# Kernel optimization log

Measured on AMD Instinct MI355X. Metric: run time of the kernel, lower is better.

## Reference

```python
import jax, jax.numpy as jnp
import numpy as np

B, N, D = 256, 128, 512
NUM_TYPES, NUM_STATS = 6, 8
W_TYPE, W_STATS, W_CORR = 1.0, 1.0, 0.5
LN_EPS = 1e-5


def setup_inputs() -> dict:
    key = jax.random.key(0)
    ks = jax.random.split(key, 20)
    s = 1.0 / np.sqrt(D)
    inp = {
        "column_embeddings": jax.random.normal(ks[0], (B, N, D), jnp.float32),
        "masked_columns": jax.random.bernoulli(ks[1], 0.15, (B, N)),
        "type_targets": jax.random.randint(ks[2], (N,), 0, NUM_TYPES),
        "column_statistics": jax.random.normal(ks[3], (B, N, NUM_STATS), jnp.float32),
        "column_correlations": jnp.tanh(jax.random.normal(ks[4], (B, N, N), jnp.float32)),
        # type head: Linear(D,D) -> GELU -> LayerNorm -> Linear(D,NUM_TYPES)
        "t_W1": jax.random.normal(ks[5], (D, D), jnp.float32) * s,
        "t_b1": jnp.zeros((D,), jnp.float32),
        "t_g": jnp.ones((D,), jnp.float32),
        "t_beta": jnp.zeros((D,), jnp.float32),
        "t_W2": jax.random.normal(ks[6], (D, NUM_TYPES), jnp.float32) * s,
        "t_b2": jnp.zeros((NUM_TYPES,), jnp.float32),
        # stats head
        "s_W1": jax.random.normal(ks[7], (D, D), jnp.float32) * s,
        "s_b1": jnp.zeros((D,), jnp.float32),
        "s_g": jnp.ones((D,), jnp.float32),
        "s_beta": jnp.zeros((D,), jnp.float32),
        "s_W2": jax.random.normal(ks[8], (D, NUM_STATS), jnp.float32) * s,
        "s_b2": jnp.zeros((NUM_STATS,), jnp.float32),
        # bilinear correlation: x_i^T W x_j + b
        "c_W": jax.random.normal(ks[9], (D, D), jnp.float32) * s,
        "c_b": jnp.zeros((), jnp.float32),
    }
    return inp


def _mlp_head(x, W1, b1, g, beta, W2, b2):
    h = jax.nn.gelu(x @ W1 + b1, approximate=False)
    mu = h.mean(-1, keepdims=True)
    var = ((h - mu) ** 2).mean(-1, keepdims=True)
    h = (h - mu) * jax.lax.rsqrt(var + LN_EPS) * g + beta
    return h @ W2 + b2


def _forward(column_embeddings, masked_columns, type_targets,
             column_statistics, column_correlations,
             t_W1, t_b1, t_g, t_beta, t_W2, t_b2,
             s_W1, s_b1, s_g, s_beta, s_W2, s_b2,
             c_W, c_b):
    e = column_embeddings  # [B,N,D]
    type_logits = _mlp_head(e, t_W1, t_b1, t_g, t_beta, t_W2, t_b2)   # [B,N,T]
    stats_preds = _mlp_head(e, s_W1, s_b1, s_g, s_beta, s_W2, s_b2)   # [B,N,S]

    # batched bilinear correlation: tanh(e_i W e_j + b), diag forced to 1
    u = jnp.einsum('bnd,de->bne', e, c_W)            # [B,N,D]
    corr = jnp.tanh(jnp.einsum('bne,bme->bnm', u, e) + c_b)  # [B,N,N]
    eye = jnp.eye(e.shape[1], dtype=corr.dtype)
    corr = corr * (1.0 - eye) + eye

    m = masked_columns.astype(jnp.float32)           # [B,N]
    n_masked = jnp.maximum(m.sum(), 1.0)

    # type loss: masked-mean cross entropy; targets broadcast over batch
    logp = jax.nn.log_softmax(type_logits, axis=-1)
    tgt = jnp.broadcast_to(type_targets[None, :], m.shape)
    ce = -jnp.take_along_axis(logp, tgt[..., None], axis=-1)[..., 0]  # [B,N]
    type_loss = (ce * m).sum() / n_masked

    # stats loss: masked-mean MSE over [B,N,S]
    se = (stats_preds - column_statistics) ** 2
    stats_loss = (se * m[..., None]).sum() / (n_masked * se.shape[-1])

    # correlation loss: mask_expanded = m_i | m_j
    me = jnp.maximum(m[:, :, None], m[:, None, :])   # [B,N,N]
    n_me = jnp.maximum(me.sum(), 1.0)
    ce2 = (corr - column_correlations) ** 2
    correlation_loss = (ce2 * me).sum() / n_me

    total = W_TYPE * type_loss + W_STATS * stats_loss + W_CORR * correlation_loss
    return total


def reference(column_embeddings, masked_columns, type_targets,
              column_statistics, column_correlations,
              t_W1, t_b1, t_g, t_beta, t_W2, t_b2,
              s_W1, s_b1, s_g, s_beta, s_W2, s_b2,
              c_W, c_b):
    return _forward(column_embeddings, masked_columns, type_targets,
                    column_statistics, column_correlations,
                    t_W1, t_b1, t_g, t_beta, t_W2, t_b2,
                    s_W1, s_b1, s_g, s_beta, s_W2, s_b2,
                    c_W, c_b)
```

## Files before the change

kernel.cpp:

```cpp
#include <hip/hip_runtime.h>
#include <math.h>

#define Bx 256
#define Nx 128
#define Dx 512
#define NTYPES 6
#define NSTATS 8
#define LN_EPS 1e-5f
#define CAP 8192

typedef __attribute__((ext_vector_type(8))) short frag8;
typedef __attribute__((ext_vector_type(4))) float f32x4;

__device__ __forceinline__ unsigned short f2bf(float f) {
    unsigned u = __float_as_uint(f);
    u += 0x7fff + ((u >> 16) & 1);
    return (unsigned short)(u >> 16);
}
__device__ __forceinline__ float bf2f(unsigned short s) {
    return __uint_as_float((unsigned)s << 16);
}

#define ASYNC16(g, l) __builtin_amdgcn_global_load_lds(                      \
    (const __attribute__((address_space(1))) void*)(g),                      \
    (__attribute__((address_space(3))) void*)(l), 16, 0, 0)

#define VWAIT(NIMM)                                                          \
    asm volatile("s_waitcnt vmcnt(" #NIMM ")" ::: "memory");                 \
    __builtin_amdgcn_sched_barrier(0);
#define BARX __builtin_amdgcn_s_barrier();

#define EB_OFF    0ULL
#define HC_OFF    33554432ULL
#define WT_OFF    67108864ULL
#define WTC_OFF   68157440ULL
#define WC_OFF    68681728ULL
#define LIST_OFF  69206016ULL
#define CNTS_OFF  69238784ULL
#define BASES_OFF 69239808ULL
#define CNTP_OFF  69240832ULL
#define ACC_OFF   69240848ULL
#define DONE_OFF  69240864ULL

__global__ __launch_bounds__(256) void k_prep(
    const float* __restrict__ e, const float* __restrict__ W0,
    const float* __restrict__ W1, const float* __restrict__ W2,
    unsigned short* __restrict__ Eb, unsigned short* __restrict__ Tcmb,
    unsigned short* __restrict__ Tc, unsigned short* __restrict__ Wc,
    const int* __restrict__ m, int* __restrict__ list,
    int* __restrict__ cnts, int* __restrict__ bases, int* cntp) {
    const int bid = blockIdx.x;
    const int t = threadIdx.x;
    if (bid < 256) {
        const int b = bid;
        const int r = b * Nx + t;
        int v = 0;
        if (t < 128) v = (m[r] != 0) ? 1 : 0;
        const unsigned long long bal = __ballot(v);
        const int wid = t >> 6, lane = t & 63;
        __shared__ int wcnt[2];
        __shared__ int base;
        if (lane == 0 && wid < 2) wcnt[wid] = __popcll(bal);
        __syncthreads();
        const int cnt = wcnt[0] + wcnt[1];
        if (t == 0) {
            base = atomicAdd(cntp, cnt);
            cnts[b] = cnt;
            bases[b] = base;
        }
        __syncthreads();
        if (t < 128 && v) {
            const int rank = __popcll(bal & ((1ULL << lane) - 1)) +
                             (wid ? wcnt[0] : 0);
            const int p = base + rank;
            if (p < CAP) list[p] = r;
        }
        return;
    }
    if (bid < 448) {
        const int lin = bid - 256;
        const int mid = lin >> 6;
        const int tl  = lin & 63;
        const int ti = tl >> 3, tj = tl & 7;
        const float* W = (mid == 0) ? W0 : (mid == 1) ? W1 : W2;
        unsigned short* T = (mid == 2) ? Tc : (Tcmb + mid * 262144);
        __shared__ float sh[64][65];
        const int c = t & 63;
        const int r4 = t >> 6;
#pragma unroll
        for (int rr = 0; rr < 16; ++rr) {
            const int row = rr * 4 + r4;
            sh[row][c] = W[(size_t)(ti * 64 + row) * Dx + tj * 64 + c];
        }
        __syncthreads();
#pragma unroll
        for (int rr = 0; rr < 16; ++rr) {
            const int col2 = rr * 4 + r4;
            T[(size_t)(tj * 64 + col2) * Dx + ti * 64 + c] = f2bf(sh[c][col2]);
        }
        return;
    }
    if (bid < 512) {
        const int base = (bid - 448) * 4096 + t * 16;
        const float4* src = (const float4*)(W2 + base);
        unsigned short o[16];
#pragma unroll
        for (int q = 0; q < 4; ++q) {
            const float4 v = src[q];
            o[q * 4 + 0] = f2bf(v.x); o[q * 4 + 1] = f2bf(v.y);
            o[q * 4 + 2] = f2bf(v.z); o[q * 4 + 3] = f2bf(v.w);
        }
        *(uint4*)(Wc + base) = *(const uint4*)(o);
        *(uint4*)(Wc + base + 8) = *(const uint4*)(o + 8);
        return;
    }
    const int r = (bid - 512) * 4 + (t >> 6);
    const int lane = t & 63;
    const float4* src = (const float4*)(e + (size_t)r * Dx);
    const float4 a = src[lane * 2];
    const float4 b = src[lane * 2 + 1];
    unsigned short u[8] = {f2bf(a.x), f2bf(a.y), f2bf(a.z), f2bf(a.w),
                           f2bf(b.x), f2bf(b.y), f2bf(b.z), f2bf(b.w)};
    ((uint4*)(Eb + (size_t)r * Dx))[lane] = *(const uint4*)u;
}

__global__ __launch_bounds__(512) void k_gemms(
    const unsigned short* __restrict__ Eb,
    const unsigned short* __restrict__ Wtcmb,
    const unsigned short* __restrict__ Wtc,
    const unsigned short* __restrict__ Wc,
    const float* __restrict__ bias0, const float* __restrict__ bias1,
    unsigned short* __restrict__ Hc,
    const int* __restrict__ list, const int* __restrict__ cntp) {
    __shared__ unsigned short As[2 * 4096];
    __shared__ unsigned short Bs[2 * 8192];
    const int bid = blockIdx.x;
    const int t = threadIdx.x;
    const int cnt = min(*cntp, CAP);
    const int rt = ((bid >> 6) << 3) | (bid & 7);
    const int row0 = rt << 7;
    if (row0 >= cnt) return;
    const int ct = (bid >> 3) & 7;
    const int col0 = ct << 8;
    const unsigned short* Bbase =
        (ct < 4) ? (Wtcmb + (size_t)ct * 256 * Dx)
      : (ct < 6) ? (Wtc + (size_t)(ct - 4) * 256 * Dx)
                 : (Wc + (size_t)(ct - 6) * 256 * Dx);
    const int kq = (t & 3) ^ ((t >> 3) & 3);
    const int ra = list[min(row0 + (t >> 2), cnt - 1)];
    const unsigned short* pA = Eb + (size_t)ra * Dx + kq * 8;
    const unsigned short* pB0 = Bbase + (size_t)(t >> 2) * Dx + kq * 8;
    const unsigned short* pB1 = pB0 + (size_t)128 * Dx;
    const int w = t >> 6, l = t & 63;
    const int wr = (w >> 2) * 64, wcol = (w & 3) * 64;
    const int quad = l >> 4, mr = l & 15;
    const int co = (quad ^ ((mr >> 1) & 3)) * 8;

#define MSTAGE(bf, k0)                                                       \
  { ASYNC16(pA + (k0), As + (bf) * 4096 + t * 8);                            \
    ASYNC16(pB0 + (k0), Bs + (bf) * 8192 + t * 8);                           \
    ASYNC16(pB1 + (k0), Bs + (bf) * 8192 + 4096 + t * 8); }

    f32x4 acc[4][4] = {};
    MSTAGE(0, 0);
    int buf = 0;
    for (int k = 0; k < 16; ++k) {
        if (k < 15) { MSTAGE(buf ^ 1, (k + 1) * 32); VWAIT(3); }
        else        { VWAIT(0); }
        BARX;
        frag8 af[4], bfv[4];
#pragma unroll
        for (int i = 0; i < 4; ++i)
            af[i] = *(const frag8*)&As[buf * 4096 + (wr + i * 16 + mr) * 32 + co];
#pragma unroll
        for (int j = 0; j < 4; ++j)
            bfv[j] = *(const frag8*)&Bs[buf * 8192 + (wcol + j * 16 + mr) * 32 + co];
        __builtin_amdgcn_s_setprio(1);
#pragma unroll
        for (int i = 0; i < 4; ++i)
#pragma unroll
            for (int j = 0; j < 4; ++j)
                acc[i][j] = __builtin_amdgcn_mfma_f32_16x16x32_bf16(
                    af[i], bfv[j], acc[i][j], 0, 0, 0);
        __builtin_amdgcn_s_setprio(0);
        if (k < 15) BARX;
        buf ^= 1;
    }
#pragma unroll
    for (int i = 0; i < 4; ++i)
#pragma unroll
        for (int j = 0; j < 4; ++j)
#pragma unroll
            for (int r = 0; r < 4; ++r) {
                const int row = row0 + wr + i * 16 + quad * 4 + r;
                const int col = col0 + wcol + j * 16 + mr;
                float v = acc[i][j][r];
                if (col < 1024) {
                    v += (col < 512) ? bias0[col] : bias1[col - 512];
                    v = 0.5f * v * (1.0f + erff(v * 0.70710678118654752f));
                }
                Hc[(size_t)row * 2048 + col] = f2bf(v);
            }
#undef MSTAGE
}

__global__ __launch_bounds__(256) void k_tail(
    const unsigned short* __restrict__ Eb,
    const float* __restrict__ Ct, const int* __restrict__ m,
    const float* __restrict__ cbp,
    const unsigned short* __restrict__ Hc,
    const float* __restrict__ tg, const float* __restrict__ tbeta,
    const float* __restrict__ tW2, const float* __restrict__ tb2,
    const float* __restrict__ sg, const float* __restrict__ sbeta,
    const float* __restrict__ sW2, const float* __restrict__ sb2,
    const int* __restrict__ list, const int* __restrict__ cnts,
    const int* __restrict__ bases, const int* __restrict__ cntp,
    const int* __restrict__ tgt, const float* __restrict__ stats,
    float* __restrict__ accs, int* __restrict__ done,
    float* __restrict__ out) {
    __shared__ unsigned short Elds[2 * 4096];
    __shared__ unsigned short Ulds[2 * 4096];
    __shared__ unsigned short Vlds[2 * 4096];
    __shared__ float mloc[128];
    __shared__ int lrow[128];
    __shared__ float redf[4][2];
    const int t = threadIdx.x;
    const int w = t >> 6, l = t & 63;
    const int quad = l >> 4, mr = l & 15;

    if (blockIdx.x < 256) {
        const int b = blockIdx.x;
        const int cnt = cnts[b];
        const int cbase = bases[b];
        const int nt = (cnt + 15) >> 4;
        if (t < 128) {
            mloc[t] = (m[b * Nx + t] != 0) ? 1.0f : 0.0f;
            lrow[t] = (t < cnt) ? (list[cbase + t] & (Nx - 1)) : 0;
        }
        __syncthreads();
        float T1 = 0.0f, T2 = 0.0f, Tov = 0.0f;
        if (cnt > 0) {
            const int kq = (t & 3) ^ ((t >> 3) & 3);
            const size_t rb = (size_t)b * Nx;
            const unsigned short* pE0 = Eb + (rb + (t >> 2)) * Dx + kq * 8;
            const unsigned short* pE1 = Eb + (rb + 64 + (t >> 2)) * Dx + kq * 8;
            const int ur0 = min((t >> 2), cnt - 1);
            const int ur1 = min(64 + (t >> 2), cnt - 1);
            const unsigned short* pU0 = Hc + (size_t)(cbase + ur0) * 2048 + 1024 + kq * 8;
            const unsigned short* pU1 = Hc + (size_t)(cbase + ur1) * 2048 + 1024 + kq * 8;
            const unsigned short* pV0 = Hc + (size_t)(cbase + ur0) * 2048 + 1536 + kq * 8;
            const unsigned short* pV1 = Hc + (size_t)(cbase + ur1) * 2048 + 1536 + kq * 8;
            const int co = (quad ^ ((mr >> 1) & 3)) * 8;

#define CSTAGE(bf, k0)                                                       \
  { ASYNC16(pE0 + (k0), Elds + (bf) * 4096 + t * 8);                         \
    ASYNC16(pE1 + (k0), Elds + (bf) * 4096 + 2048 + t * 8);                  \
    ASYNC16(pU0 + (k0), Ulds + (bf) * 4096 + t * 8);                         \
    ASYNC16(pU1 + (k0), Ulds + (bf) * 4096 + 2048 + t * 8);                  \
    ASYNC16(pV0 + (k0), Vlds + (bf) * 4096 + t * 8);                         \
    ASYNC16(pV1 + (k0), Vlds + (bf) * 4096 + 2048 + t * 8); }

            f32x4 ar[8][2] = {};
            f32x4 ac[2][8] = {};
            CSTAGE(0, 0);
            int buf = 0;
            for (int k = 0; k < 16; ++k) {
                if (k < 15) { CSTAGE(buf ^ 1, (k + 1) * 32); VWAIT(6); }
                else        { VWAIT(0); }
                BARX;
                frag8 ef[2];
#pragma unroll
                for (int eidx = 0; eidx < 2; ++eidx)
                    ef[eidx] = *(const frag8*)&Elds[buf * 4096 +
                        (w * 32 + eidx * 16 + mr) * 32 + co];
                __builtin_amdgcn_s_setprio(1);
#pragma unroll
                for (int it = 0; it < 8; ++it)
                    if (it < nt) {
                        const frag8 uf = *(const frag8*)&Ulds[buf * 4096 +
                            (it * 16 + mr) * 32 + co];
                        ar[it][0] = __builtin_amdgcn_mfma_f32_16x16x32_bf16(
                            uf, ef[0], ar[it][0], 0, 0, 0);
                        ar[it][1] = __builtin_amdgcn_mfma_f32_16x16x32_bf16(
                            uf, ef[1], ar[it][1], 0, 0, 0);
                    }
#pragma unroll
                for (int jt = 0; jt < 8; ++jt)
                    if (jt < nt) {
                        const frag8 vf = *(const frag8*)&Vlds[buf * 4096 +
                            (jt * 16 + mr) * 32 + co];
                        ac[0][jt] = __builtin_amdgcn_mfma_f32_16x16x32_bf16(
                            ef[0], vf, ac[0][jt], 0, 0, 0);
                        ac[1][jt] = __builtin_amdgcn_mfma_f32_16x16x32_bf16(
                            ef[1], vf, ac[1][jt], 0, 0, 0);
                    }
                __builtin_amdgcn_s_setprio(0);
                if (k < 15) BARX;
                buf ^= 1;
            }
            const float cb = cbp[0];
            const float* Ctb = Ct + (size_t)b * Nx * Nx;
#pragma unroll
            for (int it = 0; it < 8; ++it)
                if (it < nt) {
#pragma unroll
                    for (int eidx = 0; eidx < 2; ++eidx) {
                        const int j = w * 32 + eidx * 16 + mr;
#pragma unroll
                        for (int r = 0; r < 4; ++r) {
                            const int pos = it * 16 + quad * 4 + r;
                            if (pos < cnt) {
                                const int i = lrow[pos];
                                const float s = ar[it][eidx][r];
                                const float c = (i == j) ? 1.0f : tanhf(s + cb);
                                const float d = c - Ctb[i * Nx + j];
                                T1 += d * d;
                                Tov += d * d * mloc[j];
                            }
                        }
                    }
                }
#pragma unroll
            for (int jt = 0; jt < 8; ++jt)
                if (jt < nt) {
                    const int pos = jt * 16 + mr;
                    const int valid = (pos < cnt);
                    const int j = lrow[pos];
#pragma unroll
                    for (int eidx = 0; eidx < 2; ++eidx) {
#pragma unroll
                        for (int r = 0; r < 4; ++r) {
                            if (valid) {
                                const int i = w * 32 + eidx * 16 + quad * 4 + r;
                                const float s = ac[eidx][jt][r];
                                const float c = (i == j) ? 1.0f : tanhf(s + cb);
                                const float d = c - Ctb[i * Nx + j];
                                T2 += d * d;
                            }
                        }
                    }
                }
#undef CSTAGE
        }
        float lsum = T1 + T2 - Tov;
#pragma unroll
        for (int off = 32; off > 0; off >>= 1) lsum += __shfl_down(lsum, off);
        if (l == 0) redf[w][0] = lsum;
        __syncthreads();
        if (t == 0) {
            atomicAdd(&accs[2], redf[0][0] + redf[1][0] + redf[2][0] + redf[3][0]);
            const float c = (float)cnt;
            atomicAdd(&accs[3], 256.0f * c - c * c);
        }
    } else {
        const int blk = blockIdx.x - 256;
        const int cnt = min(*cntp, CAP);
        float ce_acc = 0.0f, sse_acc = 0.0f;
        for (int idx = blk * 4 + w; idx < cnt; idx += 256 * 4) {
            const int r = list[idx];
            const uint4 ut = ((const uint4*)(Hc + (size_t)idx * 2048))[l];
            const uint4 us = ((const uint4*)(Hc + (size_t)idx * 2048 + 512))[l];
            float a[8], b8[8];
            {
                const unsigned uu[4] = {ut.x, ut.y, ut.z, ut.w};
                const unsigned vv[4] = {us.x, us.y, us.z, us.w};
#pragma unroll
                for (int j = 0; j < 4; ++j) {
                    a[2 * j]      = bf2f((unsigned short)(uu[j] & 0xffff));
                    a[2 * j + 1]  = bf2f((unsigned short)(uu[j] >> 16));
                    b8[2 * j]     = bf2f((unsigned short)(vv[j] & 0xffff));
                    b8[2 * j + 1] = bf2f((unsigned short)(vv[j] >> 16));
                }
            }
            float st = 0, qt = 0, ss = 0, qs = 0;
#pragma unroll
            for (int j = 0; j < 8; ++j) {
                st += a[j]; qt += a[j] * a[j];
                ss += b8[j]; qs += b8[j] * b8[j];
            }
#pragma unroll
            for (int off = 32; off > 0; off >>= 1) {
                st += __shfl_xor(st, off); qt += __shfl_xor(qt, off);
                ss += __shfl_xor(ss, off); qs += __shfl_xor(qs, off);
            }
            const float mt = st * (1.0f / Dx);
            const float rt = rsqrtf(qt * (1.0f / Dx) - mt * mt + LN_EPS);
            const float ms = ss * (1.0f / Dx);
            const float rs = rsqrtf(qs * (1.0f / Dx) - ms * ms + LN_EPS);

            const int c0 = l * 8;
            float tp[6] = {}, sp[8] = {};
#pragma unroll
            for (int j = 0; j < 8; ++j) {
                const int c = c0 + j;
                const float nt2 = (a[j] - mt) * rt * tg[c] + tbeta[c];
#pragma unroll
                for (int k = 0; k < 6; ++k) tp[k] += nt2 * tW2[c * 6 + k];
                const float ns = (b8[j] - ms) * rs * sg[c] + sbeta[c];
#pragma unroll
                for (int k = 0; k < 8; ++k) sp[k] += ns * sW2[c * 8 + k];
            }
#pragma unroll
            for (int k = 0; k < 6; ++k)
#pragma unroll
                for (int off = 32; off > 0; off >>= 1) tp[k] += __shfl_down(tp[k], off);
#pragma unroll
            for (int k = 0; k < 8; ++k)
#pragma unroll
                for (int off = 32; off > 0; off >>= 1) sp[k] += __shfl_down(sp[k], off);

            if (l == 0) {
                float lg[6];
#pragma unroll
                for (int k = 0; k < 6; ++k) lg[k] = tp[k] + tb2[k];
                float mx = lg[0];
#pragma unroll
                for (int k = 1; k < 6; ++k) mx = fmaxf(mx, lg[k]);
                float se = 0.0f;
#pragma unroll
                for (int k = 0; k < 6; ++k) se += expf(lg[k] - mx);
                ce_acc += -(lg[tgt[r & (Nx - 1)]] - mx - logf(se));
                float sse = 0.0f;
#pragma unroll
                for (int k = 0; k < 8; ++k) {
                    const float d = sp[k] + sb2[k] - stats[(size_t)r * NSTATS + k];
                    sse += d * d;
                }
                sse_acc += sse;
            }
        }
        if (l == 0) { redf[w][0] = ce_acc; redf[w][1] = sse_acc; }
        __syncthreads();
        if (t == 0) {
            atomicAdd(&accs[0], redf[0][0] + redf[1][0] + redf[2][0] + redf[3][0]);
            atomicAdd(&accs[1], redf[0][1] + redf[1][1] + redf[2][1] + redf[3][1]);
        }
    }
    __syncthreads();
    if (t == 0) {
        __threadfence();
        const int old = atomicAdd(done, 1);
        if (old == 511) {
            __threadfence();
            const float CE  = atomicAdd(&accs[0], 0.0f);
            const float SSE = atomicAdd(&accs[1], 0.0f);
            const float CO  = atomicAdd(&accs[2], 0.0f);
            const float ME  = atomicAdd(&accs[3], 0.0f);
            const float nm = fmaxf((float)min(*cntp, CAP), 1.0f);
            out[0] = CE / nm + SSE / (nm * (float)NSTATS) +
                     0.5f * CO / fmaxf(ME, 1.0f);
        }
    }
}

extern "C" void kernel_launch(void* const* d_in, const int* in_sizes, int n_in,
                              void* d_out, int out_size, void* d_ws, size_t ws_size,
                              hipStream_t stream) {
    const float* e      = (const float*)d_in[0];
    const int*   mcols  = (const int*)d_in[1];
    const int*   ttgt   = (const int*)d_in[2];
    const float* stats  = (const float*)d_in[3];
    const float* corrT  = (const float*)d_in[4];
    const float* tW1    = (const float*)d_in[5];
    const float* tb1    = (const float*)d_in[6];
    const float* tg     = (const float*)d_in[7];
    const float* tbeta  = (const float*)d_in[8];
    const float* tW2    = (const float*)d_in[9];
    const float* tb2    = (const float*)d_in[10];
    const float* sW1    = (const float*)d_in[11];
    const float* sb1    = (const float*)d_in[12];
    const float* sg     = (const float*)d_in[13];
    const float* sbeta  = (const float*)d_in[14];
    const float* sW2    = (const float*)d_in[15];
    const float* sb2    = (const float*)d_in[16];
    const float* cW     = (const float*)d_in[17];
    const float* cb     = (const float*)d_in[18];
    float* out = (float*)d_out;

    char* ws = (char*)d_ws;
    unsigned short* Eb    = (unsigned short*)(ws + EB_OFF);
    unsigned short* Hc    = (unsigned short*)(ws + HC_OFF);
    unsigned short* Wtcmb = (unsigned short*)(ws + WT_OFF);
    unsigned short* Wtc   = (unsigned short*)(ws + WTC_OFF);
    unsigned short* Wc    = (unsigned short*)(ws + WC_OFF);
    int*   list  = (int*)(ws + LIST_OFF);
    int*   cnts  = (int*)(ws + CNTS_OFF);
    int*   bases = (int*)(ws + BASES_OFF);
    int*   cntp  = (int*)(ws + CNTP_OFF);
    float* accs  = (float*)(ws + ACC_OFF);
    int*   done  = (int*)(ws + DONE_OFF);

    hipMemsetAsync(ws + CNTP_OFF, 0, 48, stream);
    k_prep<<<8704, 256, 0, stream>>>(e, tW1, sW1, cW, Eb, Wtcmb, Wtc, Wc,
                                     mcols, list, cnts, bases, cntp);
    k_gemms<<<512, 512, 0, stream>>>(Eb, Wtcmb, Wtc, Wc, tb1, sb1, Hc,
                                     list, cntp);
    k_tail<<<512, 256, 0, stream>>>(Eb, corrT, mcols, cb, Hc,
                                    tg, tbeta, tW2, tb2, sg, sbeta, sW2, sb2,
                                    list, cnts, bases, cntp, ttgt, stats,
                                    accs, done, out);
}
```

Before: 238.8 us.

## Drop bf16 embedding pre-conversion; load fp32 tiles and convert in-register

Removes the prep pass that converted all 32K embedding rows to bf16, so the GEMM and tail kernels stream fp32 embeddings into LDS and convert to bf16 fragments with packed convert instructions just before the MFMAs. This avoids a full read-and-write pass over the 64MB embedding tensor, but the later kernels now read twice as many bytes for the A operand. The tail kernel also splits each batch across two blocks (768 blocks total) and moves to a three-stage LDS pipeline to raise parallelism, at the cost of reloading the U/V tiles in both halves.

```diff
diff --git a/kernel.cpp b/kernel.cpp
--- a/kernel.cpp
+++ b/kernel.cpp
@@ -21,6 +21,17 @@
     return __uint_as_float((unsigned)s << 16);
 }
 
+__device__ __forceinline__ frag8 cvt_frag8(float4 a, float4 b) {
+    unsigned r0, r1, r2, r3;
+    asm("v_cvt_pk_bf16_f32 %0, %1, %2" : "=v"(r0) : "v"(a.x), "v"(a.y));
+    asm("v_cvt_pk_bf16_f32 %0, %1, %2" : "=v"(r1) : "v"(a.z), "v"(a.w));
+    asm("v_cvt_pk_bf16_f32 %0, %1, %2" : "=v"(r2) : "v"(b.x), "v"(b.y));
+    asm("v_cvt_pk_bf16_f32 %0, %1, %2" : "=v"(r3) : "v"(b.z), "v"(b.w));
+    union { unsigned u[4]; frag8 f; } u4;
+    u4.u[0] = r0; u4.u[1] = r1; u4.u[2] = r2; u4.u[3] = r3;
+    return u4.f;
+}
+
 #define ASYNC16(g, l) __builtin_amdgcn_global_load_lds(                      \
     (const __attribute__((address_space(1))) void*)(g),                      \
     (__attribute__((address_space(3))) void*)(l), 16, 0, 0)
@@ -30,23 +41,22 @@
     __builtin_amdgcn_sched_barrier(0);
 #define BARX __builtin_amdgcn_s_barrier();
 
-#define EB_OFF    0ULL
-#define HC_OFF    33554432ULL
-#define WT_OFF    67108864ULL
-#define WTC_OFF   68157440ULL
-#define WC_OFF    68681728ULL
-#define LIST_OFF  69206016ULL
-#define CNTS_OFF  69238784ULL
-#define BASES_OFF 69239808ULL
-#define CNTP_OFF  69240832ULL
-#define ACC_OFF   69240848ULL
-#define DONE_OFF  69240864ULL
+#define HC_OFF    0ULL
+#define WT_OFF    33554432ULL
+#define WTC_OFF   34603008ULL
+#define WC_OFF    35127296ULL
+#define LIST_OFF  35651584ULL
+#define CNTS_OFF  35684352ULL
+#define BASES_OFF 35685376ULL
+#define CNTP_OFF  35686400ULL
+#define ACC_OFF   35686416ULL
+#define DONE_OFF  35686432ULL
 
 __global__ __launch_bounds__(256) void k_prep(
-    const float* __restrict__ e, const float* __restrict__ W0,
-    const float* __restrict__ W1, const float* __restrict__ W2,
-    unsigned short* __restrict__ Eb, unsigned short* __restrict__ Tcmb,
-    unsigned short* __restrict__ Tc, unsigned short* __restrict__ Wc,
+    const float* __restrict__ W0, const float* __restrict__ W1,
+    const float* __restrict__ W2,
+    unsigned short* __restrict__ Tcmb, unsigned short* __restrict__ Tc,
+    unsigned short* __restrict__ Wc,
     const int* __restrict__ m, int* __restrict__ list,
     int* __restrict__ cnts, int* __restrict__ bases, int* cntp) {
     const int bid = blockIdx.x;
@@ -100,40 +110,29 @@
         }
         return;
     }
-    if (bid < 512) {
-        const int base = (bid - 448) * 4096 + t * 16;
-        const float4* src = (const float4*)(W2 + base);
-        unsigned short o[16];
-#pragma unroll
-        for (int q = 0; q < 4; ++q) {
-            const float4 v = src[q];
-            o[q * 4 + 0] = f2bf(v.x); o[q * 4 + 1] = f2bf(v.y);
-            o[q * 4 + 2] = f2bf(v.z); o[q * 4 + 3] = f2bf(v.w);
-        }
-        *(uint4*)(Wc + base) = *(const uint4*)(o);
-        *(uint4*)(Wc + base + 8) = *(const uint4*)(o + 8);
-        return;
+    const int base = (bid - 448) * 4096 + t * 16;
+    const float4* src = (const float4*)(W2 + base);
+    unsigned short o[16];
+#pragma unroll
+    for (int q = 0; q < 4; ++q) {
+        const float4 v = src[q];
+        o[q * 4 + 0] = f2bf(v.x); o[q * 4 + 1] = f2bf(v.y);
+        o[q * 4 + 2] = f2bf(v.z); o[q * 4 + 3] = f2bf(v.w);
     }
-    const int r = (bid - 512) * 4 + (t >> 6);
-    const int lane = t & 63;
-    const float4* src = (const float4*)(e + (size_t)r * Dx);
-    const float4 a = src[lane * 2];
-    const float4 b = src[lane * 2 + 1];
-    unsigned short u[8] = {f2bf(a.x), f2bf(a.y), f2bf(a.z), f2bf(a.w),
-                           f2bf(b.x), f2bf(b.y), f2bf(b.z), f2bf(b.w)};
-    ((uint4*)(Eb + (size_t)r * Dx))[lane] = *(const uint4*)u;
+    *(uint4*)(Wc + base) = *(const uint4*)(o);
+    *(uint4*)(Wc + base + 8) = *(const uint4*)(o + 8);
 }
 
 __global__ __launch_bounds__(512) void k_gemms(
-    const unsigned short* __restrict__ Eb,
+    const float* __restrict__ e,
     const unsigned short* __restrict__ Wtcmb,
     const unsigned short* __restrict__ Wtc,
     const unsigned short* __restrict__ Wc,
     const float* __restrict__ bias0, const float* __restrict__ bias1,
     unsigned short* __restrict__ Hc,
     const int* __restrict__ list, const int* __restrict__ cntp) {
-    __shared__ unsigned short As[2 * 4096];
-    __shared__ unsigned short Bs[2 * 8192];
+    __shared__ float Af[2 * 4096];
+    __shared__ unsigned short Bsh[2 * 8192];
     const int bid = blockIdx.x;
     const int t = threadIdx.x;
     const int cnt = min(*cntp, CAP);
@@ -146,35 +145,45 @@
         (ct < 4) ? (Wtcmb + (size_t)ct * 256 * Dx)
       : (ct < 6) ? (Wtc + (size_t)(ct - 4) * 256 * Dx)
                  : (Wc + (size_t)(ct - 6) * 256 * Dx);
-    const int kq = (t & 3) ^ ((t >> 3) & 3);
-    const int ra = list[min(row0 + (t >> 2), cnt - 1)];
-    const unsigned short* pA = Eb + (size_t)ra * Dx + kq * 8;
-    const unsigned short* pB0 = Bbase + (size_t)(t >> 2) * Dx + kq * 8;
-    const unsigned short* pB1 = pB0 + (size_t)128 * Dx;
+    const int kqA = ((t & 7) ^ ((t >> 3) & 7)) * 4;
+    const int ra0 = list[min(row0 + (t >> 3), cnt - 1)];
+    const int ra1 = list[min(row0 + 64 + (t >> 3), cnt - 1)];
+    const float* pA0 = e + (size_t)ra0 * Dx + kqA;
+    const float* pA1 = e + (size_t)ra1 * Dx + kqA;
+    const int kqB = (t & 3) ^ ((t >> 3) & 3);
+    const unsigned short* pB0 = Bbase + (size_t)(t >> 2) * Dx + kqB * 8;
+    const unsigned short* pB1 = Bbase + (size_t)(128 + (t >> 2)) * Dx + kqB * 8;
     const int w = t >> 6, l = t & 63;
     const int wr = (w >> 2) * 64, wcol = (w & 3) * 64;
     const int quad = l >> 4, mr = l & 15;
     const int co = (quad ^ ((mr >> 1) & 3)) * 8;
-
-#define MSTAGE(bf, k0)                                                       \
-  { ASYNC16(pA + (k0), As + (bf) * 4096 + t * 8);                            \
-    ASYNC16(pB0 + (k0), Bs + (bf) * 8192 + t * 8);                           \
-    ASYNC16(pB1 + (k0), Bs + (bf) * 8192 + 4096 + t * 8); }
+    const int xA = mr & 7;
+    const int s0 = (quad * 2) ^ xA;
+
+#define MSTAGE(bf, kk)                                                       \
+  { ASYNC16(pA0 + (kk) * 32, Af + (bf) * 4096 + t * 4);                      \
+    ASYNC16(pA1 + (kk) * 32, Af + (bf) * 4096 + 2048 + t * 4);               \
+    ASYNC16(pB0 + (kk) * 32, Bsh + (bf) * 8192 + t * 8);                     \
+    ASYNC16(pB1 + (kk) * 32, Bsh + (bf) * 8192 + 4096 + t * 8); }
 
     f32x4 acc[4][4] = {};
     MSTAGE(0, 0);
     int buf = 0;
     for (int k = 0; k < 16; ++k) {
-        if (k < 15) { MSTAGE(buf ^ 1, (k + 1) * 32); VWAIT(3); }
+        if (k < 15) { MSTAGE(buf ^ 1, k + 1); VWAIT(4); }
         else        { VWAIT(0); }
         BARX;
         frag8 af[4], bfv[4];
 #pragma unroll
-        for (int i = 0; i < 4; ++i)
-            af[i] = *(const frag8*)&As[buf * 4096 + (wr + i * 16 + mr) * 32 + co];
+        for (int i = 0; i < 4; ++i) {
+            const int lr = wr + i * 16 + mr;
+            const float4 lo = *(const float4*)&Af[buf * 4096 + lr * 32 + s0 * 4];
+            const float4 hi = *(const float4*)&Af[buf * 4096 + lr * 32 + (s0 ^ 1) * 4];
+            af[i] = cvt_frag8(lo, hi);
+        }
 #pragma unroll
         for (int j = 0; j < 4; ++j)
-            bfv[j] = *(const frag8*)&Bs[buf * 8192 + (wcol + j * 16 + mr) * 32 + co];
+            bfv[j] = *(const frag8*)&Bsh[buf * 8192 + (wcol + j * 16 + mr) * 32 + co];
         __builtin_amdgcn_s_setprio(1);
 #pragma unroll
         for (int i = 0; i < 4; ++i)
@@ -205,7 +214,7 @@
 }
 
 __global__ __launch_bounds__(256) void k_tail(
-    const unsigned short* __restrict__ Eb,
+    const float* __restrict__ e,
     const float* __restrict__ Ct, const int* __restrict__ m,
     const float* __restrict__ cbp,
     const unsigned short* __restrict__ Hc,
@@ -218,9 +227,9 @@
     const int* __restrict__ tgt, const float* __restrict__ stats,
     float* __restrict__ accs, int* __restrict__ done,
     float* __restrict__ out) {
-    __shared__ unsigned short Elds[2 * 4096];
-    __shared__ unsigned short Ulds[2 * 4096];
-    __shared__ unsigned short Vlds[2 * 4096];
+    __shared__ float Ef[3 * 2048];
+    __shared__ unsigned short Ulds[3 * 4096];
+    __shared__ unsigned short Vlds[3 * 4096];
     __shared__ float mloc[128];
     __shared__ int lrow[128];
     __shared__ float redf[4][2];
@@ -228,8 +237,9 @@
     const int w = t >> 6, l = t & 63;
     const int quad = l >> 4, mr = l & 15;
 
-    if (blockIdx.x < 256) {
-        const int b = blockIdx.x;
+    if (blockIdx.x < 512) {
+        const int b = blockIdx.x >> 1;
+        const int h = blockIdx.x & 1;
         const int cnt = cnts[b];
         const int cbase = bases[b];
         const int nt = (cnt + 15) >> 4;
@@ -240,10 +250,11 @@
         __syncthreads();
         float T1 = 0.0f, T2 = 0.0f, Tov = 0.0f;
         if (cnt > 0) {
+            const int kqE = ((t & 7) ^ ((t >> 3) & 7)) * 4;
+            const size_t rb = (size_t)b * Nx + h * 64;
+            const float* pE0 = e + (rb + (t >> 3)) * Dx + kqE;
+            const float* pE1 = e + (rb + 32 + (t >> 3)) * Dx + kqE;
             const int kq = (t & 3) ^ ((t >> 3) & 3);
-            const size_t rb = (size_t)b * Nx;
-            const unsigned short* pE0 = Eb + (rb + (t >> 2)) * Dx + kq * 8;
-            const unsigned short* pE1 = Eb + (rb + 64 + (t >> 2)) * Dx + kq * 8;
             const int ur0 = min((t >> 2), cnt - 1);
             const int ur1 = min(64 + (t >> 2), cnt - 1);
             const unsigned short* pU0 = Hc + (size_t)(cbase + ur0) * 2048 + 1024 + kq * 8;
@@ -251,72 +262,65 @@
             const unsigned short* pV0 = Hc + (size_t)(cbase + ur0) * 2048 + 1536 + kq * 8;
             const unsigned short* pV1 = Hc + (size_t)(cbase + ur1) * 2048 + 1536 + kq * 8;
             const int co = (quad ^ ((mr >> 1) & 3)) * 8;
-
-#define CSTAGE(bf, k0)                                                       \
-  { ASYNC16(pE0 + (k0), Elds + (bf) * 4096 + t * 8);                         \
-    ASYNC16(pE1 + (k0), Elds + (bf) * 4096 + 2048 + t * 8);                  \
-    ASYNC16(pU0 + (k0), Ulds + (bf) * 4096 + t * 8);                         \
-    ASYNC16(pU1 + (k0), Ulds + (bf) * 4096 + 2048 + t * 8);                  \
-    ASYNC16(pV0 + (k0), Vlds + (bf) * 4096 + t * 8);                         \
-    ASYNC16(pV1 + (k0), Vlds + (bf) * 4096 + 2048 + t * 8); }
-
-            f32x4 ar[8][2] = {};
-            f32x4 ac[2][8] = {};
-            CSTAGE(0, 0);
-            int buf = 0;
+            const int xE = mr & 7;
+            const int se0 = (quad * 2) ^ xE;
+
+#define CSTAGE(bf, ph)                                                       \
+  { ASYNC16(pE0 + (ph) * 32, Ef + (bf) * 2048 + t * 4);                      \
+    ASYNC16(pE1 + (ph) * 32, Ef + (bf) * 2048 + 1024 + t * 4);               \
+    ASYNC16(pU0 + (ph) * 32, Ulds + (bf) * 4096 + t * 8);                    \
+    ASYNC16(pU1 + (ph) * 32, Ulds + (bf) * 4096 + 2048 + t * 8);             \
+    ASYNC16(pV0 + (ph) * 32, Vlds + (bf) * 4096 + t * 8);                    \
+    ASYNC16(pV1 + (ph) * 32, Vlds + (bf) * 4096 + 2048 + t * 8); }
+
+            f32x4 ar[8] = {};
+            f32x4 ac[8] = {};
+            CSTAGE(0, 0); CSTAGE(1, 1);
             for (int k = 0; k < 16; ++k) {
-                if (k < 15) { CSTAGE(buf ^ 1, (k + 1) * 32); VWAIT(6); }
-                else        { VWAIT(0); }
+                if (k < 15) { VWAIT(6); } else { VWAIT(0); }
                 BARX;
-                frag8 ef[2];
-#pragma unroll
-                for (int eidx = 0; eidx < 2; ++eidx)
-                    ef[eidx] = *(const frag8*)&Elds[buf * 4096 +
-                        (w * 32 + eidx * 16 + mr) * 32 + co];
+                if (k < 14) CSTAGE((k + 2) % 3, k + 2);
+                const int buf = k % 3;
+                const int lre = w * 16 + mr;
+                const float4 lo = *(const float4*)&Ef[buf * 2048 + lre * 32 + se0 * 4];
+                const float4 hi = *(const float4*)&Ef[buf * 2048 + lre * 32 + (se0 ^ 1) * 4];
+                const frag8 ef = cvt_frag8(lo, hi);
                 __builtin_amdgcn_s_setprio(1);
 #pragma unroll
                 for (int it = 0; it < 8; ++it)
                     if (it < nt) {
                         const frag8 uf = *(const frag8*)&Ulds[buf * 4096 +
                             (it * 16 + mr) * 32 + co];
-                        ar[it][0] = __builtin_amdgcn_mfma_f32_16x16x32_bf16(
-                            uf, ef[0], ar[it][0], 0, 0, 0);
-                        ar[it][1] = __builtin_amdgcn_mfma_f32_16x16x32_bf16(
-                            uf, ef[1], ar[it][1], 0, 0, 0);
+                        ar[it] = __builtin_amdgcn_mfma_f32_16x16x32_bf16(
+                            uf, ef, ar[it], 0, 0, 0);
                     }
 #pragma unroll
                 for (int jt = 0; jt < 8; ++jt)
                     if (jt < nt) {
                         const frag8 vf = *(const frag8*)&Vlds[buf * 4096 +
                             (jt * 16 + mr) * 32 + co];
-                        ac[0][jt] = __builtin_amdgcn_mfma_f32_16x16x32_bf16(
-                            ef[0], vf, ac[0][jt], 0, 0, 0);
-                        ac[1][jt] = __builtin_amdgcn_mfma_f32_16x16x32_bf16(
-                            ef[1], vf, ac[1][jt], 0, 0, 0);
+                        ac[jt] = __builtin_amdgcn_mfma_f32_16x16x32_bf16(
+                            ef, vf, ac[jt], 0, 0, 0);
                     }
                 __builtin_amdgcn_s_setprio(0);
                 if (k < 15) BARX;
-                buf ^= 1;
             }
             const float cb = cbp[0];
             const float* Ctb = Ct + (size_t)b * Nx * Nx;
+            const int j1 = h * 64 + w * 16 + mr;
 #pragma unroll
             for (int it = 0; it < 8; ++it)
                 if (it < nt) {
 #pragma unroll
-                    for (int eidx = 0; eidx < 2; ++eidx) {
-                        const int j = w * 32 + eidx * 16 + mr;
-#pragma unroll
-                        for (int r = 0; r < 4; ++r) {
-                            const int pos = it * 16 + quad * 4 + r;
-                            if (pos < cnt) {
-                                const int i = lrow[pos];
-                                const float s = ar[it][eidx][r];
-                                const float c = (i == j) ? 1.0f : tanhf(s + cb);
-                                const float d = c - Ctb[i * Nx + j];
-                                T1 += d * d;
-                                Tov += d * d * mloc[j];
-                            }
+                    for (int r = 0; r < 4; ++r) {
+                        const int pos = it * 16 + quad * 4 + r;
+                        if (pos < cnt) {
+                            const int i = lrow[pos];
+                            const float s = ar[it][r];
+                            const float c = (i == j1) ? 1.0f : tanhf(s + cb);
+                            const float d = c - Ctb[i * Nx + j1];
+                            T1 += d * d;
+                            Tov += d * d * mloc[j1];
                         }
                     }
                 }
@@ -327,16 +331,13 @@
                     const int valid = (pos < cnt);
                     const int j = lrow[pos];
 #pragma unroll
-                    for (int eidx = 0; eidx < 2; ++eidx) {
-#pragma unroll
-                        for (int r = 0; r < 4; ++r) {
-                            if (valid) {
-                                const int i = w * 32 + eidx * 16 + quad * 4 + r;
-                                const float s = ac[eidx][jt][r];
-                                const float c = (i == j) ? 1.0f : tanhf(s + cb);
-                                const float d = c - Ctb[i * Nx + j];
-                                T2 += d * d;
-                            }
+                    for (int r = 0; r < 4; ++r) {
+                        if (valid) {
+                            const int i = h * 64 + w * 16 + quad * 4 + r;
+                            const float s = ac[jt][r];
+                            const float c = (i == j) ? 1.0f : tanhf(s + cb);
+                            const float d = c - Ctb[i * Nx + j];
+                            T2 += d * d;
                         }
                     }
                 }
@@ -349,11 +350,13 @@
         __syncthreads();
         if (t == 0) {
             atomicAdd(&accs[2], redf[0][0] + redf[1][0] + redf[2][0] + redf[3][0]);
-            const float c = (float)cnt;
-            atomicAdd(&accs[3], 256.0f * c - c * c);
+            if (h == 0) {
+                const float c = (float)cnt;
+                atomicAdd(&accs[3], 256.0f * c - c * c);
+            }
         }
     } else {
-        const int blk = blockIdx.x - 256;
+        const int blk = blockIdx.x - 512;
         const int cnt = min(*cntp, CAP);
         float ce_acc = 0.0f, sse_acc = 0.0f;
         for (int idx = blk * 4 + w; idx < cnt; idx += 256 * 4) {
@@ -440,7 +443,7 @@
     if (t == 0) {
         __threadfence();
         const int old = atomicAdd(done, 1);
-        if (old == 511) {
+        if (old == 767) {
             __threadfence();
             const float CE  = atomicAdd(&accs[0], 0.0f);
             const float SSE = atomicAdd(&accs[1], 0.0f);
@@ -478,7 +481,6 @@
     float* out = (float*)d_out;
 
     char* ws = (char*)d_ws;
-    unsigned short* Eb    = (unsigned short*)(ws + EB_OFF);
     unsigned short* Hc    = (unsigned short*)(ws + HC_OFF);
     unsigned short* Wtcmb = (unsigned short*)(ws + WT_OFF);
     unsigned short* Wtc   = (unsigned short*)(ws + WTC_OFF);
@@ -491,11 +493,11 @@
     int*   done  = (int*)(ws + DONE_OFF);
 
     hipMemsetAsync(ws + CNTP_OFF, 0, 48, stream);
-    k_prep<<<8704, 256, 0, stream>>>(e, tW1, sW1, cW, Eb, Wtcmb, Wtc, Wc,
-                                     mcols, list, cnts, bases, cntp);
-    k_gemms<<<512, 512, 0, stream>>>(Eb, Wtcmb, Wtc, Wc, tb1, sb1, Hc,
+    k_prep<<<512, 256, 0, stream>>>(tW1, sW1, cW, Wtcmb, Wtc, Wc,
+                                    mcols, list, cnts, bases, cntp);
+    k_gemms<<<512, 512, 0, stream>>>(e, Wtcmb, Wtc, Wc, tb1, sb1, Hc,
                                      list, cntp);
-    k_tail<<<512, 256, 0, stream>>>(Eb, corrT, mcols, cb, Hc,
+    k_tail<<<768, 256, 0, stream>>>(e, corrT, mcols, cb, Hc,
                                     tg, tbeta, tW2, tb2, sg, sbeta, sW2, sb2,
                                     list, cnts, bases, cntp, ttgt, stats,
                                     accs, done, out);
```

Result: slower. 557.5 us (+133.5%).

## Chunk masked-column correlation tiles by 32 to cut accumulators and LDS

Applied to the files above, without the earlier changes.

The correlation tail kernel used to hold accumulators for up to 128 masked columns at once (8x2 plus 2x8 MFMA tiles) and staged full U/V tiles in LDS. It now processes masked columns in chunks of 32, with smaller accumulator arrays, a quarter of the U/V LDS footprint, and U and V loads split across the two half-blocks. The aim is lower register and LDS pressure, which should allow higher occupancy. The cost is that the E tile is re-streamed from global memory once per chunk, adding loads and barriers when a batch has many masked columns.

```diff
diff --git a/kernel.cpp b/kernel.cpp
--- a/kernel.cpp
+++ b/kernel.cpp
@@ -219,8 +219,8 @@
     float* __restrict__ accs, int* __restrict__ done,
     float* __restrict__ out) {
     __shared__ unsigned short Elds[2 * 4096];
-    __shared__ unsigned short Ulds[2 * 4096];
-    __shared__ unsigned short Vlds[2 * 4096];
+    __shared__ unsigned short Ulds[2 * 1024];
+    __shared__ unsigned short Vlds[2 * 1024];
     __shared__ float mloc[128];
     __shared__ int lrow[128];
     __shared__ float redf[4][2];
@@ -232,115 +232,118 @@
         const int b = blockIdx.x;
         const int cnt = cnts[b];
         const int cbase = bases[b];
-        const int nt = (cnt + 15) >> 4;
         if (t < 128) {
             mloc[t] = (m[b * Nx + t] != 0) ? 1.0f : 0.0f;
             lrow[t] = (t < cnt) ? (list[cbase + t] & (Nx - 1)) : 0;
         }
         __syncthreads();
         float T1 = 0.0f, T2 = 0.0f, Tov = 0.0f;
+        const float cb = cbp[0];
+        const float* Ctb = Ct + (size_t)b * Nx * Nx;
         if (cnt > 0) {
             const int kq = (t & 3) ^ ((t >> 3) & 3);
             const size_t rb = (size_t)b * Nx;
             const unsigned short* pE0 = Eb + (rb + (t >> 2)) * Dx + kq * 8;
             const unsigned short* pE1 = Eb + (rb + 64 + (t >> 2)) * Dx + kq * 8;
-            const int ur0 = min((t >> 2), cnt - 1);
-            const int ur1 = min(64 + (t >> 2), cnt - 1);
-            const unsigned short* pU0 = Hc + (size_t)(cbase + ur0) * 2048 + 1024 + kq * 8;
-            const unsigned short* pU1 = Hc + (size_t)(cbase + ur1) * 2048 + 1024 + kq * 8;
-            const unsigned short* pV0 = Hc + (size_t)(cbase + ur0) * 2048 + 1536 + kq * 8;
-            const unsigned short* pV1 = Hc + (size_t)(cbase + ur1) * 2048 + 1536 + kq * 8;
             const int co = (quad ^ ((mr >> 1) & 3)) * 8;
-
-#define CSTAGE(bf, k0)                                                       \
-  { ASYNC16(pE0 + (k0), Elds + (bf) * 4096 + t * 8);                         \
-    ASYNC16(pE1 + (k0), Elds + (bf) * 4096 + 2048 + t * 8);                  \
-    ASYNC16(pU0 + (k0), Ulds + (bf) * 4096 + t * 8);                         \
-    ASYNC16(pU1 + (k0), Ulds + (bf) * 4096 + 2048 + t * 8);                  \
-    ASYNC16(pV0 + (k0), Vlds + (bf) * 4096 + t * 8);                         \
-    ASYNC16(pV1 + (k0), Vlds + (bf) * 4096 + 2048 + t * 8); }
-
-            f32x4 ar[8][2] = {};
-            f32x4 ac[2][8] = {};
-            CSTAGE(0, 0);
-            int buf = 0;
-            for (int k = 0; k < 16; ++k) {
-                if (k < 15) { CSTAGE(buf ^ 1, (k + 1) * 32); VWAIT(6); }
-                else        { VWAIT(0); }
-                BARX;
-                frag8 ef[2];
-#pragma unroll
-                for (int eidx = 0; eidx < 2; ++eidx)
-                    ef[eidx] = *(const frag8*)&Elds[buf * 4096 +
-                        (w * 32 + eidx * 16 + mr) * 32 + co];
-                __builtin_amdgcn_s_setprio(1);
-#pragma unroll
-                for (int it = 0; it < 8; ++it)
-                    if (it < nt) {
-                        const frag8 uf = *(const frag8*)&Ulds[buf * 4096 +
-                            (it * 16 + mr) * 32 + co];
-                        ar[it][0] = __builtin_amdgcn_mfma_f32_16x16x32_bf16(
-                            uf, ef[0], ar[it][0], 0, 0, 0);
-                        ar[it][1] = __builtin_amdgcn_mfma_f32_16x16x32_bf16(
-                            uf, ef[1], ar[it][1], 0, 0, 0);
-                    }
-#pragma unroll
-                for (int jt = 0; jt < 8; ++jt)
-                    if (jt < nt) {
-                        const frag8 vf = *(const frag8*)&Vlds[buf * 4096 +
-                            (jt * 16 + mr) * 32 + co];
-                        ac[0][jt] = __builtin_amdgcn_mfma_f32_16x16x32_bf16(
-                            ef[0], vf, ac[0][jt], 0, 0, 0);
-                        ac[1][jt] = __builtin_amdgcn_mfma_f32_16x16x32_bf16(
-                            ef[1], vf, ac[1][jt], 0, 0, 0);
-                    }
-                __builtin_amdgcn_s_setprio(0);
-                if (k < 15) BARX;
-                buf ^= 1;
-            }
-            const float cb = cbp[0];
-            const float* Ctb = Ct + (size_t)b * Nx * Nx;
-#pragma unroll
-            for (int it = 0; it < 8; ++it)
-                if (it < nt) {
-#pragma unroll
-                    for (int eidx = 0; eidx < 2; ++eidx) {
-                        const int j = w * 32 + eidx * 16 + mr;
-#pragma unroll
-                        for (int r = 0; r < 4; ++r) {
-                            const int pos = it * 16 + quad * 4 + r;
-                            if (pos < cnt) {
-                                const int i = lrow[pos];
-                                const float s = ar[it][eidx][r];
-                                const float c = (i == j) ? 1.0f : tanhf(s + cb);
-                                const float d = c - Ctb[i * Nx + j];
-                                T1 += d * d;
-                                Tov += d * d * mloc[j];
+            const int hw = t >> 7;
+            const int t2 = t & 127;
+
+            for (int c0 = 0; c0 < cnt; c0 += 32) {
+                const int ntc = min(((cnt - c0) + 15) >> 4, 2);
+                const int urow = min(c0 + (t2 >> 2), cnt - 1);
+                const unsigned short* pUV = Hc + (size_t)(cbase + urow) * 2048
+                                            + (hw ? 1536 : 1024) + kq * 8;
+                unsigned short* UVdst = hw ? Vlds : Ulds;
+
+#define TSTAGE(bf, ph)                                                       \
+  { ASYNC16(pE0 + (ph) * 32, Elds + (bf) * 4096 + t * 8);                    \
+    ASYNC16(pE1 + (ph) * 32, Elds + (bf) * 4096 + 2048 + t * 8);             \
+    ASYNC16(pUV + (ph) * 32, UVdst + (bf) * 1024 + t2 * 8); }
+
+                f32x4 ar[2][2] = {};
+                f32x4 ac[2][2] = {};
+                TSTAGE(0, 0);
+                int buf = 0;
+                for (int k = 0; k < 16; ++k) {
+                    if (k < 15) { TSTAGE(buf ^ 1, k + 1); VWAIT(3); }
+                    else        { VWAIT(0); }
+                    BARX;
+                    frag8 ef[2];
+#pragma unroll
+                    for (int eidx = 0; eidx < 2; ++eidx)
+                        ef[eidx] = *(const frag8*)&Elds[buf * 4096 +
+                            (w * 32 + eidx * 16 + mr) * 32 + co];
+                    __builtin_amdgcn_s_setprio(1);
+#pragma unroll
+                    for (int it = 0; it < 2; ++it)
+                        if (it < ntc) {
+                            const frag8 uf = *(const frag8*)&Ulds[buf * 1024 +
+                                (it * 16 + mr) * 32 + co];
+                            ar[it][0] = __builtin_amdgcn_mfma_f32_16x16x32_bf16(
+                                uf, ef[0], ar[it][0], 0, 0, 0);
+                            ar[it][1] = __builtin_amdgcn_mfma_f32_16x16x32_bf16(
+                                uf, ef[1], ar[it][1], 0, 0, 0);
+                        }
+#pragma unroll
+                    for (int jt = 0; jt < 2; ++jt)
+                        if (jt < ntc) {
+                            const frag8 vf = *(const frag8*)&Vlds[buf * 1024 +
+                                (jt * 16 + mr) * 32 + co];
+                            ac[0][jt] = __builtin_amdgcn_mfma_f32_16x16x32_bf16(
+                                ef[0], vf, ac[0][jt], 0, 0, 0);
+                            ac[1][jt] = __builtin_amdgcn_mfma_f32_16x16x32_bf16(
+                                ef[1], vf, ac[1][jt], 0, 0, 0);
+                        }
+                    __builtin_amdgcn_s_setprio(0);
+                    if (k < 15) BARX;
+                    buf ^= 1;
+                }
+#pragma unroll
+                for (int it = 0; it < 2; ++it)
+                    if (it < ntc) {
+#pragma unroll
+                        for (int eidx = 0; eidx < 2; ++eidx) {
+                            const int j = w * 32 + eidx * 16 + mr;
+#pragma unroll
+                            for (int r = 0; r < 4; ++r) {
+                                const int pos = c0 + it * 16 + quad * 4 + r;
+                                if (pos < cnt) {
+                                    const int i = lrow[pos];
+                                    const float s = ar[it][eidx][r];
+                                    const float c = (i == j) ? 1.0f
+                                                             : tanhf(s + cb);
+                                    const float d = c - Ctb[i * Nx + j];
+                                    T1 += d * d;
+                                    Tov += d * d * mloc[j];
+                                }
                             }
                         }
                     }
-                }
-#pragma unroll
-            for (int jt = 0; jt < 8; ++jt)
-                if (jt < nt) {
-                    const int pos = jt * 16 + mr;
-                    const int valid = (pos < cnt);
-                    const int j = lrow[pos];
-#pragma unroll
-                    for (int eidx = 0; eidx < 2; ++eidx) {
-#pragma unroll
-                        for (int r = 0; r < 4; ++r) {
-                            if (valid) {
-                                const int i = w * 32 + eidx * 16 + quad * 4 + r;
-                                const float s = ac[eidx][jt][r];
-                                const float c = (i == j) ? 1.0f : tanhf(s + cb);
-                                const float d = c - Ctb[i * Nx + j];
-                                T2 += d * d;
+#pragma unroll
+                for (int jt = 0; jt < 2; ++jt)
+                    if (jt < ntc) {
+                        const int pos = c0 + jt * 16 + mr;
+                        const int valid = (pos < cnt);
+                        const int j = lrow[pos & 127];
+#pragma unroll
+                        for (int eidx = 0; eidx < 2; ++eidx) {
+#pragma unroll
+                            for (int r = 0; r < 4; ++r) {
+                                if (valid) {
+                                    const int i = w * 32 + eidx * 16 +
+                                                  quad * 4 + r;
+                                    const float s = ac[eidx][jt][r];
+                                    const float c = (i == j) ? 1.0f
+                                                             : tanhf(s + cb);
+                                    const float d = c - Ctb[i * Nx + j];
+                                    T2 += d * d;
+                                }
                             }
                         }
                     }
-                }
-#undef CSTAGE
+#undef TSTAGE
+            }
         }
         float lsum = T1 + T2 - Tov;
 #pragma unroll
```

Measured after the change: 226.0 us. -5.4%, faster.
